# Performance work log

Measured on AMD Instinct MI355X. Metric: run time of the kernel, lower is better.

The kernel has to match this reference:

```python
import jax, jax.numpy as jnp
import numpy as np

D, H, L, P, DFF = 256, 8, 4, 4, 512
HD = D // H
SHAPES = [(128, 128), (64, 64), (32, 32), (16, 16)]


def setup_inputs() -> dict:
    key = jax.random.key(0)
    ks = jax.random.split(key, 16)
    N, Lq = 8, 1000
    Lin = sum(h * w for h, w in SHAPES)
    f = lambda k, s, sc=1.0: jax.random.normal(k, s, dtype=jnp.float32) * sc
    starts = np.cumsum([0] + [h * w for h, w in SHAPES[:-1]])
    return {
        "pre_tgt": f(ks[0], (N, Lq, D)),
        "pre_query_pos": f(ks[1], (N, Lq, D)),
        "src": f(ks[2], (N, Lin, D)),
        "pre_ref_pts": jax.random.uniform(ks[3], (N, Lq, L, 2), dtype=jnp.float32),
        "src_padding_mask": jnp.zeros((N, Lin), dtype=bool),
        "src_spatial_shapes": jnp.array(SHAPES, dtype=jnp.int32),
        "level_start_index": jnp.array(starts, dtype=jnp.int32),
        "W_value": f(ks[4], (D, D), 0.02), "b_value": jnp.zeros((D,), jnp.float32),
        "W_off": f(ks[5], (D, H * L * P * 2), 0.01), "b_off": f(ks[6], (H * L * P * 2,), 0.1),
        "W_attn": f(ks[7], (D, H * L * P), 0.02), "b_attn": jnp.zeros((H * L * P,), jnp.float32),
        "W_out": f(ks[8], (D, D), 0.02), "b_out": jnp.zeros((D,), jnp.float32),
        "g1": jnp.ones((D,), jnp.float32), "be1": jnp.zeros((D,), jnp.float32),
        "W1": f(ks[9], (D, DFF), 0.02), "b1": jnp.zeros((DFF,), jnp.float32),
        "W2": f(ks[10], (DFF, D), 0.02), "b2": jnp.zeros((D,), jnp.float32),
        "g3": jnp.ones((D,), jnp.float32), "be3": jnp.zeros((D,), jnp.float32),
    }


def layernorm(x, g, b):
    m = x.mean(-1, keepdims=True)
    v = x.var(-1, keepdims=True)
    return (x - m) * jax.lax.rsqrt(v + 1e-5) * g + b


def msdeform_attn(query, ref_pts, src, pad_mask, shapes_np,
                  W_value, b_value, W_off, b_off, W_attn, b_attn, W_out, b_out):
    N, Lq, _ = query.shape
    value = src @ W_value + b_value
    value = jnp.where(pad_mask[..., None], 0.0, value)
    value = value.reshape(N, -1, H, HD)
    off = (query @ W_off + b_off).reshape(N, Lq, H, L, P, 2)
    attn = jax.nn.softmax((query @ W_attn + b_attn).reshape(N, Lq, H, L * P), -1)
    attn = attn.reshape(N, Lq, H, L, P)
    # offset normalizer is (W, H) per level
    norm = jnp.asarray(shapes_np[:, [1, 0]], dtype=query.dtype)  # [L,2]
    loc = ref_pts[:, :, None, :, None, :] + off / norm[None, None, None, :, None, :]
    out = jnp.zeros((N, Lq, H, HD), dtype=query.dtype)
    n_idx = jnp.arange(N)[:, None, None, None]
    h_idx = jnp.arange(H)[None, None, :, None]
    start = 0
    for l in range(L):
        Hl, Wl = int(shapes_np[l, 0]), int(shapes_np[l, 1])
        vl = value[:, start:start + Hl * Wl].reshape(N, Hl, Wl, H, HD)
        start += Hl * Wl
        # grid_sample align_corners=False: pixel = loc*size - 0.5, zero padding
        x = loc[:, :, :, l, :, 0] * Wl - 0.5  # [N,Lq,H,P]
        y = loc[:, :, :, l, :, 1] * Hl - 0.5
        x0 = jnp.floor(x); y0 = jnp.floor(y)
        fx = x - x0; fy = y - y0
        x0i = x0.astype(jnp.int32); y0i = y0.astype(jnp.int32)
        samp = jnp.zeros(x.shape + (HD,), dtype=value.dtype)
        for dx, wx in ((0, 1.0 - fx), (1, fx)):
            for dy, wy in ((0, 1.0 - fy), (1, fy)):
                xi = x0i + dx; yi = y0i + dy
                valid = (xi >= 0) & (xi < Wl) & (yi >= 0) & (yi < Hl)
                v = vl[n_idx, jnp.clip(yi, 0, Hl - 1), jnp.clip(xi, 0, Wl - 1), h_idx]
                samp = samp + jnp.where(valid, wx * wy, 0.0)[..., None] * v
        out = out + jnp.einsum('nqhp,nqhpd->nqhd', attn[:, :, :, l], samp)
    return out.reshape(N, Lq, D) @ W_out + b_out


def reference(pre_tgt, pre_query_pos, src, pre_ref_pts, src_padding_mask,
              src_spatial_shapes, level_start_index,
              W_value, b_value, W_off, b_off, W_attn, b_attn, W_out, b_out,
              g1, be1, W1, b1, W2, b2, g3, be3):
    shapes_np = np.asarray(src_spatial_shapes)
    q = pre_tgt + pre_query_pos
    attn_out = msdeform_attn(q, pre_ref_pts, src, src_padding_mask, shapes_np,
                             W_value, b_value, W_off, b_off, W_attn, b_attn, W_out, b_out)
    tgt = layernorm(pre_tgt + attn_out, g1, be1)  # dropout=identity (eval)
    ff = jax.nn.relu(tgt @ W1 + b1) @ W2 + b2
    return layernorm(tgt + ff, g3, be3)
```

## Files before the change

### kernel.cpp

```cpp
#include <hip/hip_runtime.h>
#include <hip/hip_bf16.h>

#define D_MODEL 256
#define NHEAD   8
#define NLEV    4
#define NPTS    4
#define HDIM    32
#define DFFN    512
#define NBATCH  8
#define LQ      1000
#define LIN     21760
#define M_VAL   (NBATCH * LIN)
#define M_Q     (NBATCH * LQ)

typedef __attribute__((ext_vector_type(8))) short short8;
typedef __attribute__((ext_vector_type(4))) short short4v;
typedef __attribute__((ext_vector_type(4))) float f32x4;

struct alignas(8) bf16x4 { __hip_bfloat16 a, b, c, d; };

__device__ __forceinline__ short f2bf(float f) {
    __hip_bfloat16 h = __float2bfloat16(f);
    return *reinterpret_cast<short*>(&h);
}

__global__ __launch_bounds__(256)
void transpose_weights_kernel(const float* __restrict__ Wv, const float* __restrict__ Wo,
                              const float* __restrict__ W1, const float* __restrict__ W2,
                              short* __restrict__ Wv_t, short* __restrict__ Wo_t,
                              short* __restrict__ W1_t, short* __restrict__ W2_t)
{
    const int b = blockIdx.x;
    const float* src; short* dst; int K, N, tb;
    if (b < 64)       { src = Wv; dst = Wv_t; K = 256; N = 256; tb = b; }
    else if (b < 128) { src = Wo; dst = Wo_t; K = 256; N = 256; tb = b - 64; }
    else if (b < 256) { src = W1; dst = W1_t; K = 256; N = 512; tb = b - 128; }
    else              { src = W2; dst = W2_t; K = 512; N = 256; tb = b - 256; }
    const int ntn = N >> 5;
    const int kt = tb / ntn, nt = tb % ntn;
    __shared__ float t[32][33];
    const int x = threadIdx.x & 31, y = threadIdx.x >> 5;
    #pragma unroll
    for (int j = 0; j < 4; ++j)
        t[y + 8*j][x] = src[(kt*32 + y + 8*j) * N + nt*32 + x];
    __syncthreads();
    #pragma unroll
    for (int j = 0; j < 4; ++j)
        dst[(nt*32 + y + 8*j) * K + kt*32 + x] = f2bf(t[x][y + 8*j]);
}

#define BM 64
#define BN 128
#define BK 64

template<bool A_BF16, bool RELU, bool MASK, bool OUT_BF16>
__global__ __launch_bounds__(256)
void mfma_gemm_kernel(const void* __restrict__ Ain,
                      const short* __restrict__ Bt,
                      const float* __restrict__ bias,
                      const unsigned char* __restrict__ mask,
                      float* __restrict__ C, __hip_bfloat16* __restrict__ Cb,
                      int M, int N, int K)
{
    __shared__ short As[BM * BK];
    __shared__ short Bs[BN * BK];
    const int tid  = threadIdx.x;
    const int lane = tid & 63, wid = tid >> 6;
    const int wr = wid >> 1, wc = wid & 1;
    const long bm = (long)blockIdx.y * BM;
    const int  bn = blockIdx.x * BN;

    f32x4 acc[2][4];
    #pragma unroll
    for (int m = 0; m < 2; ++m)
        #pragma unroll
        for (int n = 0; n < 4; ++n)
            acc[m][n] = (f32x4){0.f, 0.f, 0.f, 0.f};

    const int ar  = tid >> 2;
    const int akq = (tid & 3) * 16;
    const int brn = tid >> 1;
    const int bkq = (tid & 1) * 32;

    for (int k0 = 0; k0 < K; k0 += BK) {
        if (!A_BF16) {
            const float* Ap = (const float*)Ain + (bm + ar) * (long)K + k0 + akq;
            #pragma unroll
            for (int i = 0; i < 4; ++i) {
                float4 v = *reinterpret_cast<const float4*>(Ap + 4*i);
                short4v s;
                s[0] = f2bf(v.x); s[1] = f2bf(v.y); s[2] = f2bf(v.z); s[3] = f2bf(v.w);
                const int e = (akq + 4*i) ^ ((ar & 7) << 3);
                *reinterpret_cast<short4v*>(&As[ar * BK + e]) = s;
            }
        } else {
            const short* Ap = (const short*)Ain + (bm + ar) * (long)K + k0 + akq;
            #pragma unroll
            for (int i = 0; i < 2; ++i) {
                short8 v = *reinterpret_cast<const short8*>(Ap + 8*i);
                const int e = (akq + 8*i) ^ ((ar & 7) << 3);
                *reinterpret_cast<short8*>(&As[ar * BK + e]) = v;
            }
        }
        {
            const short* Bp = Bt + (bn + brn) * (long)K + k0 + bkq;
            #pragma unroll
            for (int i = 0; i < 4; ++i) {
                short8 v = *reinterpret_cast<const short8*>(Bp + 8*i);
                const int e = (bkq + 8*i) ^ ((brn & 7) << 3);
                *reinterpret_cast<short8*>(&Bs[brn * BK + e]) = v;
            }
        }
        __syncthreads();
        #pragma unroll
        for (int kk = 0; kk < 2; ++kk) {
            const int kb = kk * 32 + (lane >> 4) * 8;
            short8 af[2], bfr[4];
            #pragma unroll
            for (int m = 0; m < 2; ++m) {
                const int row = wr * 32 + m * 16 + (lane & 15);
                af[m] = *reinterpret_cast<const short8*>(&As[row * BK + (kb ^ ((row & 7) << 3))]);
            }
            #pragma unroll
            for (int n = 0; n < 4; ++n) {
                const int row = wc * 64 + n * 16 + (lane & 15);
                bfr[n] = *reinterpret_cast<const short8*>(&Bs[row * BK + (kb ^ ((row & 7) << 3))]);
            }
            #pragma unroll
            for (int m = 0; m < 2; ++m)
                #pragma unroll
                for (int n = 0; n < 4; ++n)
                    acc[m][n] = __builtin_amdgcn_mfma_f32_16x16x32_bf16(af[m], bfr[n], acc[m][n], 0, 0, 0);
        }
        __syncthreads();
    }

    #pragma unroll
    for (int m = 0; m < 2; ++m) {
        #pragma unroll
        for (int n = 0; n < 4; ++n) {
            const int col = bn + wc * 64 + n * 16 + (lane & 15);
            const float bc = bias[col];
            #pragma unroll
            for (int r = 0; r < 4; ++r) {
                const long row = bm + wr * 32 + m * 16 + (lane >> 4) * 4 + r;
                float v = acc[m][n][r] + bc;
                if (RELU) v = fmaxf(v, 0.f);
                if (MASK) { if (mask[row]) v = 0.f; }
                if (OUT_BF16) Cb[row * (long)N + col] = __float2bfloat16(v);
                else          C[row * (long)N + col]  = v;
            }
        }
    }
}

template<bool ADD_A2>
__global__ __launch_bounds__(256)
void gemm_kernel(const float* __restrict__ A, const float* __restrict__ A2,
                 const float* __restrict__ B, const float* __restrict__ bias,
                 float* __restrict__ C, int M, int N, int K)
{
    __shared__ float As[16][68];
    __shared__ float Bs[16][64];
    const int tid = threadIdx.x;
    const long bm = (long)blockIdx.y * 64;
    const int  bn = blockIdx.x * 64;
    const int  tx = tid & 15, ty = tid >> 4;
    const int  ar = tid >> 2, ac = (tid & 3) * 4;

    float acc[4][4] = {};
    const float* Aptr  = A + (bm + ar) * (long)K + ac;
    const float* A2ptr = ADD_A2 ? (A2 + (bm + ar) * (long)K + ac) : nullptr;
    const float* Bptr  = B + (long)ty * N + bn + tx * 4;

    for (int k0 = 0; k0 < K; k0 += 16) {
        float4 av = *reinterpret_cast<const float4*>(Aptr + k0);
        if (ADD_A2) {
            float4 a2 = *reinterpret_cast<const float4*>(A2ptr + k0);
            av.x += a2.x; av.y += a2.y; av.z += a2.z; av.w += a2.w;
        }
        float4 bv = *reinterpret_cast<const float4*>(Bptr + (long)k0 * N);
        As[ac + 0][ar] = av.x; As[ac + 1][ar] = av.y;
        As[ac + 2][ar] = av.z; As[ac + 3][ar] = av.w;
        *reinterpret_cast<float4*>(&Bs[ty][tx * 4]) = bv;
        __syncthreads();
        #pragma unroll
        for (int kk = 0; kk < 16; ++kk) {
            float4 a4 = *reinterpret_cast<const float4*>(&As[kk][ty * 4]);
            float4 b4 = *reinterpret_cast<const float4*>(&Bs[kk][tx * 4]);
            float a[4] = {a4.x, a4.y, a4.z, a4.w};
            float b[4] = {b4.x, b4.y, b4.z, b4.w};
            #pragma unroll
            for (int i = 0; i < 4; ++i)
                #pragma unroll
                for (int j = 0; j < 4; ++j)
                    acc[i][j] = fmaf(a[i], b[j], acc[i][j]);
        }
        __syncthreads();
    }
    const float4 bias4 = *reinterpret_cast<const float4*>(bias + bn + tx * 4);
    #pragma unroll
    for (int i = 0; i < 4; ++i) {
        const long row = bm + ty * 4 + i;
        const long off = row * N + bn + tx * 4;
        *reinterpret_cast<float4*>(C + off) = make_float4(
            acc[i][0] + bias4.x, acc[i][1] + bias4.y,
            acc[i][2] + bias4.z, acc[i][3] + bias4.w);
    }
}

__global__ __launch_bounds__(128)
void msdeform_sample_kernel(const float* __restrict__ off,
                            const float* __restrict__ logits,
                            const float* __restrict__ ref_pts,
                            const __hip_bfloat16* __restrict__ value,
                            __hip_bfloat16* __restrict__ samp)
{
    const int qi = blockIdx.x;
    const int n  = qi / LQ;
    const int t  = threadIdx.x;

    __shared__ int   s_idx[128][4];
    __shared__ float s_w[128][4];

    {
        const int h = t >> 4, lp = t & 15, l = lp >> 2;
        const float lg = logits[qi * 128 + t];
        float mx = lg;
        #pragma unroll
        for (int m = 1; m < 16; m <<= 1) mx = fmaxf(mx, __shfl_xor(mx, m, 64));
        const float e = __expf(lg - mx);
        float s = e;
        #pragma unroll
        for (int m = 1; m < 16; m <<= 1) s += __shfl_xor(s, m, 64);
        const float w = e / s;

        const int Wl = 128 >> l;
        constexpr int Start[4] = {0, 16384, 20480, 21504};
        const float x = ref_pts[qi * 8 + l * 2 + 0] * (float)Wl - 0.5f
                      + off[qi * 256 + h * 32 + lp * 2 + 0];
        const float y = ref_pts[qi * 8 + l * 2 + 1] * (float)Wl - 0.5f
                      + off[qi * 256 + h * 32 + lp * 2 + 1];
        const float x0f = floorf(x), y0f = floorf(y);
        const float fx = x - x0f, fy = y - y0f;
        const int x0 = (int)x0f, y0 = (int)y0f;
        const int base = n * LIN + Start[l];
        #pragma unroll
        for (int tap = 0; tap < 4; ++tap) {
            const int dx = tap & 1, dy = tap >> 1;
            const int xi = x0 + dx, yi = y0 + dy;
            const bool ok = ((unsigned)xi < (unsigned)Wl) & ((unsigned)yi < (unsigned)Wl);
            const float tw = ok ? w * (dx ? fx : 1.f - fx) * (dy ? fy : 1.f - fy) : 0.f;
            const int idx = ok ? ((base + yi * Wl + xi) * D_MODEL + h * HDIM) : 0;
            s_idx[t][tap] = idx;
            s_w[t][tap]   = tw;
        }
    }
    __syncthreads();

    {
        const int h = t >> 4, cp = t & 15;
        float a0 = 0.f, a1 = 0.f;
        #pragma unroll
        for (int lp = 0; lp < 16; ++lp) {
            const int4   i4 = *reinterpret_cast<const int4*>(s_idx[h * 16 + lp]);
            const float4 w4 = *reinterpret_cast<const float4*>(s_w[h * 16 + lp]);
            const int   idx[4] = {i4.x, i4.y, i4.z, i4.w};
            const float wt[4]  = {w4.x, w4.y, w4.z, w4.w};
            #pragma unroll
            for (int tap = 0; tap < 4; ++tap) {
                __hip_bfloat162 v2 = *reinterpret_cast<const __hip_bfloat162*>(
                    value + idx[tap] + cp * 2);
                a0 = fmaf(wt[tap], __bfloat162float(v2.x), a0);
                a1 = fmaf(wt[tap], __bfloat162float(v2.y), a1);
            }
        }
        __hip_bfloat162 o;
        o.x = __float2bfloat16(a0);
        o.y = __float2bfloat16(a1);
        *reinterpret_cast<__hip_bfloat162*>(samp + (long)qi * D_MODEL + h * HDIM + cp * 2) = o;
    }
}

__global__ __launch_bounds__(256)
void add_ln_kernel(const float* __restrict__ x, const float* __restrict__ y,
                   const float* __restrict__ g, const float* __restrict__ b,
                   float* __restrict__ out)
{
    const int row  = blockIdx.x * 4 + (threadIdx.x >> 6);
    const int lane = threadIdx.x & 63;
    const long base = (long)row * D_MODEL + lane * 4;

    float4 xv = *reinterpret_cast<const float4*>(x + base);
    float4 yv = *reinterpret_cast<const float4*>(y + base);
    float4 v  = make_float4(xv.x + yv.x, xv.y + yv.y, xv.z + yv.z, xv.w + yv.w);

    float sum = v.x + v.y + v.z + v.w;
    float sq  = v.x * v.x + v.y * v.y + v.z * v.z + v.w * v.w;
    #pragma unroll
    for (int m = 1; m < 64; m <<= 1) {
        sum += __shfl_xor(sum, m, 64);
        sq  += __shfl_xor(sq,  m, 64);
    }
    const float mean = sum * (1.f / D_MODEL);
    const float var  = sq * (1.f / D_MODEL) - mean * mean;
    const float rstd = rsqrtf(var + 1e-5f);

    float4 gv = *reinterpret_cast<const float4*>(g + lane * 4);
    float4 bv = *reinterpret_cast<const float4*>(b + lane * 4);
    float4 o;
    o.x = (v.x - mean) * rstd * gv.x + bv.x;
    o.y = (v.y - mean) * rstd * gv.y + bv.y;
    o.z = (v.z - mean) * rstd * gv.z + bv.z;
    o.w = (v.w - mean) * rstd * gv.w + bv.w;
    *reinterpret_cast<float4*>(out + base) = o;
}

extern "C" void kernel_launch(void* const* d_in, const int* in_sizes, int n_in,
                              void* d_out, int out_size, void* d_ws, size_t ws_size,
                              hipStream_t stream)
{
    const float* pre_tgt  = (const float*)d_in[0];
    const float* pre_qpos = (const float*)d_in[1];
    const float* src      = (const float*)d_in[2];
    const float* ref_pts  = (const float*)d_in[3];
    const unsigned char* pad_mask = (const unsigned char*)d_in[4];
    const float* W_value = (const float*)d_in[7];
    const float* b_value = (const float*)d_in[8];
    const float* W_off   = (const float*)d_in[9];
    const float* b_off   = (const float*)d_in[10];
    const float* W_attn  = (const float*)d_in[11];
    const float* b_attn  = (const float*)d_in[12];
    const float* W_out   = (const float*)d_in[13];
    const float* b_out   = (const float*)d_in[14];
    const float* g1      = (const float*)d_in[15];
    const float* be1     = (const float*)d_in[16];
    const float* W1      = (const float*)d_in[17];
    const float* b1      = (const float*)d_in[18];
    const float* W2      = (const float*)d_in[19];
    const float* b2      = (const float*)d_in[20];
    const float* g3      = (const float*)d_in[21];
    const float* be3     = (const float*)d_in[22];
    float* out = (float*)d_out;

    char* w = (char*)d_ws;
    size_t o = 0;
    __hip_bfloat16* value = (__hip_bfloat16*)(w + o); o += (size_t)M_VAL * D_MODEL * 2;
    float* offb    = (float*)(w + o); o += (size_t)M_Q * 256 * 4;
    float* logits  = (float*)(w + o); o += (size_t)M_Q * 128 * 4;
    __hip_bfloat16* samp = (__hip_bfloat16*)(w + o); o += (size_t)M_Q * 256 * 2;
    float* tgt     = (float*)(w + o); o += (size_t)M_Q * 256 * 4;
    short* Wv_t    = (short*)(w + o); o += 256 * 256 * 2;
    short* Wo_t    = (short*)(w + o); o += 256 * 256 * 2;
    short* W1_t    = (short*)(w + o); o += 512 * 256 * 2;
    short* W2_t    = (short*)(w + o); o += 256 * 512 * 2;
    float* attn_out = (float*)w;
    float* hidden_f_unused = nullptr; (void)hidden_f_unused;
    __hip_bfloat16* hidden = (__hip_bfloat16*)(w + 20000000);
    float* ff = offb;

    const dim3 blk(256);

    transpose_weights_kernel<<<dim3(384), blk, 0, stream>>>(
        W_value, W_out, W1, W2, Wv_t, Wo_t, W1_t, W2_t);

    mfma_gemm_kernel<false, false, true, true><<<dim3(2, M_VAL / BM), blk, 0, stream>>>(
        src, Wv_t, b_value, pad_mask, nullptr, value, M_VAL, 256, 256);

    gemm_kernel<true><<<dim3(4, M_Q / 64), blk, 0, stream>>>(
        pre_tgt, pre_qpos, W_off, b_off, offb, M_Q, 256, 256);

    gemm_kernel<true><<<dim3(2, M_Q / 64), blk, 0, stream>>>(
        pre_tgt, pre_qpos, W_attn, b_attn, logits, M_Q, 128, 256);

    msdeform_sample_kernel<<<dim3(M_Q), dim3(128), 0, stream>>>(
        offb, logits, ref_pts, value, samp);

    mfma_gemm_kernel<true, false, false, false><<<dim3(2, M_Q / BM), blk, 0, stream>>>(
        samp, Wo_t, b_out, nullptr, attn_out, nullptr, M_Q, 256, 256);

    add_ln_kernel<<<dim3(M_Q / 4), blk, 0, stream>>>(pre_tgt, attn_out, g1, be1, tgt);

    mfma_gemm_kernel<false, true, false, true><<<dim3(4, M_Q / BM), blk, 0, stream>>>(
        tgt, W1_t, b1, nullptr, nullptr, hidden, M_Q, 512, 256);

    mfma_gemm_kernel<true, false, false, false><<<dim3(2, M_Q / BM), blk, 0, stream>>>(
        hidden, W2_t, b2, nullptr, ff, nullptr, M_Q, 256, 512);

    add_ln_kernel<<<dim3(M_Q / 4), blk, 0, stream>>>(tgt, ff, g3, be3, out);
}
```

Measured before the change: 434.4 us.

## Head-major value layout, clamped bilinear gather, fused offset/attn GEMM, register prefetch

The value projection now writes a head-major layout [H][N*Lin][32], so each head's samples sit in a contiguous region. The sampling kernel clamps the 2x2 footprint inside the level and folds out-of-range taps into zero weights, which gives two contiguous 8-byte loads per point instead of four scattered 4-byte ones. The offset and attention-logit fp32 GEMMs are merged into one launch, and both GEMM kernels prefetch the next K tile into registers while computing the current one. The risks are higher register pressure, strided bf16 stores in the value GEMM epilogue, and extra branching in the weight setup.

```diff
diff --git a/kernel.cpp b/kernel.cpp
--- a/kernel.cpp
+++ b/kernel.cpp
@@ -23,6 +23,9 @@
     __hip_bfloat16 h = __float2bfloat16(f);
     return *reinterpret_cast<short*>(&h);
 }
+__device__ __forceinline__ float bf2f(short s) {
+    return __uint_as_float(((unsigned)(unsigned short)s) << 16);
+}
 
 __global__ __launch_bounds__(256)
 void transpose_weights_kernel(const float* __restrict__ Wv, const float* __restrict__ Wo,
@@ -53,7 +56,7 @@
 #define BN 128
 #define BK 64
 
-template<bool A_BF16, bool RELU, bool MASK, bool OUT_BF16>
+template<bool A_BF16, bool RELU, bool MASK, int OMODE>
 __global__ __launch_bounds__(256)
 void mfma_gemm_kernel(const void* __restrict__ Ain,
                       const short* __restrict__ Bt,
@@ -82,36 +85,52 @@
     const int brn = tid >> 1;
     const int bkq = (tid & 1) * 32;
 
-    for (int k0 = 0; k0 < K; k0 += BK) {
+    float4 a_f[4];
+    short8 a_h[2];
+    short8 b_r[4];
+
+    auto load_tile = [&](int k0) {
         if (!A_BF16) {
             const float* Ap = (const float*)Ain + (bm + ar) * (long)K + k0 + akq;
             #pragma unroll
+            for (int i = 0; i < 4; ++i)
+                a_f[i] = *reinterpret_cast<const float4*>(Ap + 4*i);
+        } else {
+            const short* Ap = (const short*)Ain + (bm + ar) * (long)K + k0 + akq;
+            #pragma unroll
+            for (int i = 0; i < 2; ++i)
+                a_h[i] = *reinterpret_cast<const short8*>(Ap + 8*i);
+        }
+        const short* Bp = Bt + (bn + brn) * (long)K + k0 + bkq;
+        #pragma unroll
+        for (int i = 0; i < 4; ++i)
+            b_r[i] = *reinterpret_cast<const short8*>(Bp + 8*i);
+    };
+    auto store_tile = [&]() {
+        if (!A_BF16) {
+            #pragma unroll
             for (int i = 0; i < 4; ++i) {
-                float4 v = *reinterpret_cast<const float4*>(Ap + 4*i);
                 short4v s;
-                s[0] = f2bf(v.x); s[1] = f2bf(v.y); s[2] = f2bf(v.z); s[3] = f2bf(v.w);
-                const int e = (akq + 4*i) ^ ((ar & 7) << 3);
-                *reinterpret_cast<short4v*>(&As[ar * BK + e]) = s;
+                s[0] = f2bf(a_f[i].x); s[1] = f2bf(a_f[i].y);
+                s[2] = f2bf(a_f[i].z); s[3] = f2bf(a_f[i].w);
+                *reinterpret_cast<short4v*>(&As[ar * BK + ((akq + 4*i) ^ ((ar & 7) << 3))]) = s;
             }
         } else {
-            const short* Ap = (const short*)Ain + (bm + ar) * (long)K + k0 + akq;
-            #pragma unroll
-            for (int i = 0; i < 2; ++i) {
-                short8 v = *reinterpret_cast<const short8*>(Ap + 8*i);
-                const int e = (akq + 8*i) ^ ((ar & 7) << 3);
-                *reinterpret_cast<short8*>(&As[ar * BK + e]) = v;
-            }
-        }
-        {
-            const short* Bp = Bt + (bn + brn) * (long)K + k0 + bkq;
-            #pragma unroll
-            for (int i = 0; i < 4; ++i) {
-                short8 v = *reinterpret_cast<const short8*>(Bp + 8*i);
-                const int e = (bkq + 8*i) ^ ((brn & 7) << 3);
-                *reinterpret_cast<short8*>(&Bs[brn * BK + e]) = v;
-            }
-        }
+            #pragma unroll
+            for (int i = 0; i < 2; ++i)
+                *reinterpret_cast<short8*>(&As[ar * BK + ((akq + 8*i) ^ ((ar & 7) << 3))]) = a_h[i];
+        }
+        #pragma unroll
+        for (int i = 0; i < 4; ++i)
+            *reinterpret_cast<short8*>(&Bs[brn * BK + ((bkq + 8*i) ^ ((brn & 7) << 3))]) = b_r[i];
+    };
+
+    load_tile(0);
+    const int nsteps = K / BK;
+    for (int s = 0; s < nsteps; ++s) {
+        store_tile();
         __syncthreads();
+        if (s + 1 < nsteps) load_tile((s + 1) * BK);
         #pragma unroll
         for (int kk = 0; kk < 2; ++kk) {
             const int kb = kk * 32 + (lane >> 4) * 8;
@@ -147,43 +166,54 @@
                 float v = acc[m][n][r] + bc;
                 if (RELU) v = fmaxf(v, 0.f);
                 if (MASK) { if (mask[row]) v = 0.f; }
-                if (OUT_BF16) Cb[row * (long)N + col] = __float2bfloat16(v);
-                else          C[row * (long)N + col]  = v;
+                if (OMODE == 0)      C[row * (long)N + col] = v;
+                else if (OMODE == 1) Cb[row * (long)N + col] = __float2bfloat16(v);
+                else {
+                    Cb[(size_t)(col >> 5) * ((size_t)M_VAL * HDIM)
+                       + (size_t)row * HDIM + (col & 31)] = __float2bfloat16(v);
+                }
             }
         }
     }
 }
 
-template<bool ADD_A2>
 __global__ __launch_bounds__(256)
-void gemm_kernel(const float* __restrict__ A, const float* __restrict__ A2,
-                 const float* __restrict__ B, const float* __restrict__ bias,
-                 float* __restrict__ C, int M, int N, int K)
+void proj_gemm_kernel(const float* __restrict__ A, const float* __restrict__ A2,
+                      const float* __restrict__ Wo, const float* __restrict__ bo,
+                      const float* __restrict__ Wa, const float* __restrict__ ba,
+                      float* __restrict__ Co, float* __restrict__ Ca)
 {
     __shared__ float As[16][68];
     __shared__ float Bs[16][64];
     const int tid = threadIdx.x;
     const long bm = (long)blockIdx.y * 64;
     const int  bn = blockIdx.x * 64;
-    const int  tx = tid & 15, ty = tid >> 4;
-    const int  ar = tid >> 2, ac = (tid & 3) * 4;
-
+    const float* B; const float* bias; float* C; int Nc, cb;
+    if (bn < 256) { B = Wo; bias = bo; C = Co; Nc = 256; cb = bn; }
+    else          { B = Wa; bias = ba; C = Ca; Nc = 128; cb = bn - 256; }
+
+    const int tx = tid & 15, ty = tid >> 4;
+    const int ar = tid >> 2, ac = (tid & 3) * 4;
     float acc[4][4] = {};
-    const float* Aptr  = A + (bm + ar) * (long)K + ac;
-    const float* A2ptr = ADD_A2 ? (A2 + (bm + ar) * (long)K + ac) : nullptr;
-    const float* Bptr  = B + (long)ty * N + bn + tx * 4;
-
-    for (int k0 = 0; k0 < K; k0 += 16) {
-        float4 av = *reinterpret_cast<const float4*>(Aptr + k0);
-        if (ADD_A2) {
-            float4 a2 = *reinterpret_cast<const float4*>(A2ptr + k0);
-            av.x += a2.x; av.y += a2.y; av.z += a2.z; av.w += a2.w;
-        }
-        float4 bv = *reinterpret_cast<const float4*>(Bptr + (long)k0 * N);
-        As[ac + 0][ar] = av.x; As[ac + 1][ar] = av.y;
-        As[ac + 2][ar] = av.z; As[ac + 3][ar] = av.w;
+    const float* Aptr = A  + (bm + ar) * 256L + ac;
+    const float* A2p  = A2 + (bm + ar) * 256L + ac;
+    const float* Bptr = B + (long)ty * Nc + cb + tx * 4;
+
+    float4 av, a2, bv;
+    auto load = [&](int k0) {
+        av = *reinterpret_cast<const float4*>(Aptr + k0);
+        a2 = *reinterpret_cast<const float4*>(A2p + k0);
+        bv = *reinterpret_cast<const float4*>(Bptr + (long)k0 * Nc);
+    };
+    load(0);
+    for (int k0 = 0; k0 < 256; k0 += 16) {
+        As[ac + 0][ar] = av.x + a2.x;
+        As[ac + 1][ar] = av.y + a2.y;
+        As[ac + 2][ar] = av.z + a2.z;
+        As[ac + 3][ar] = av.w + a2.w;
         *reinterpret_cast<float4*>(&Bs[ty][tx * 4]) = bv;
         __syncthreads();
+        if (k0 + 16 < 256) load(k0 + 16);
         #pragma unroll
         for (int kk = 0; kk < 16; ++kk) {
             float4 a4 = *reinterpret_cast<const float4*>(&As[kk][ty * 4]);
@@ -198,12 +228,11 @@
         }
         __syncthreads();
     }
-    const float4 bias4 = *reinterpret_cast<const float4*>(bias + bn + tx * 4);
+    const float4 bias4 = *reinterpret_cast<const float4*>(bias + cb + tx * 4);
     #pragma unroll
     for (int i = 0; i < 4; ++i) {
         const long row = bm + ty * 4 + i;
-        const long off = row * N + bn + tx * 4;
-        *reinterpret_cast<float4*>(C + off) = make_float4(
+        *reinterpret_cast<float4*>(C + row * Nc + cb + tx * 4) = make_float4(
             acc[i][0] + bias4.x, acc[i][1] + bias4.y,
             acc[i][2] + bias4.z, acc[i][3] + bias4.w);
     }
@@ -220,8 +249,9 @@
     const int n  = qi / LQ;
     const int t  = threadIdx.x;
 
-    __shared__ int   s_idx[128][4];
-    __shared__ float s_w[128][4];
+    __shared__ int   s_base[128];
+    __shared__ float s_wx[128][2];
+    __shared__ float s_wy[128][2];
 
     {
         const int h = t >> 4, lp = t & 15, l = lp >> 2;
@@ -230,10 +260,10 @@
         #pragma unroll
         for (int m = 1; m < 16; m <<= 1) mx = fmaxf(mx, __shfl_xor(mx, m, 64));
         const float e = __expf(lg - mx);
-        float s = e;
-        #pragma unroll
-        for (int m = 1; m < 16; m <<= 1) s += __shfl_xor(s, m, 64);
-        const float w = e / s;
+        float ssum = e;
+        #pragma unroll
+        for (int m = 1; m < 16; m <<= 1) ssum += __shfl_xor(ssum, m, 64);
+        const float w = e / ssum;
 
         const int Wl = 128 >> l;
         constexpr int Start[4] = {0, 16384, 20480, 21504};
@@ -241,44 +271,51 @@
                       + off[qi * 256 + h * 32 + lp * 2 + 0];
         const float y = ref_pts[qi * 8 + l * 2 + 1] * (float)Wl - 0.5f
                       + off[qi * 256 + h * 32 + lp * 2 + 1];
-        const float x0f = floorf(x), y0f = floorf(y);
-        const float fx = x - x0f, fy = y - y0f;
-        const int x0 = (int)x0f, y0 = (int)y0f;
-        const int base = n * LIN + Start[l];
-        #pragma unroll
-        for (int tap = 0; tap < 4; ++tap) {
-            const int dx = tap & 1, dy = tap >> 1;
-            const int xi = x0 + dx, yi = y0 + dy;
-            const bool ok = ((unsigned)xi < (unsigned)Wl) & ((unsigned)yi < (unsigned)Wl);
-            const float tw = ok ? w * (dx ? fx : 1.f - fx) * (dy ? fy : 1.f - fy) : 0.f;
-            const int idx = ok ? ((base + yi * Wl + xi) * D_MODEL + h * HDIM) : 0;
-            s_idx[t][tap] = idx;
-            s_w[t][tap]   = tw;
-        }
+        const float xf = floorf(x), yf = floorf(y);
+        const float fx = x - xf, fy = y - yf;
+        const int x0 = (int)xf, y0 = (int)yf;
+        const int xb = min(max(x0, 0), Wl - 2);
+        const int yb = min(max(y0, 0), Wl - 2);
+        const float wx0 = (xb == x0) ? (1.f - fx) : ((xb == x0 + 1) ? fx : 0.f);
+        const float wx1 = (xb + 1 == x0) ? (1.f - fx) : ((xb == x0) ? fx : 0.f);
+        const float wy0 = w * ((yb == y0) ? (1.f - fy) : ((yb == y0 + 1) ? fy : 0.f));
+        const float wy1 = w * ((yb + 1 == y0) ? (1.f - fy) : ((yb == y0) ? fy : 0.f));
+
+        const int row = n * LIN + Start[l] + yb * Wl + xb;
+        s_base[t]  = (h * M_VAL + row) * HDIM;
+        s_wx[t][0] = wx0; s_wx[t][1] = wx1;
+        s_wy[t][0] = wy0; s_wy[t][1] = wy1;
     }
     __syncthreads();
 
     {
         const int h = t >> 4, cp = t & 15;
-        float a0 = 0.f, a1 = 0.f;
+        const int side = cp >> 3, ch4 = (cp & 7) * 4;
+        float a0 = 0.f, a1 = 0.f, a2 = 0.f, a3 = 0.f;
         #pragma unroll
         for (int lp = 0; lp < 16; ++lp) {
-            const int4   i4 = *reinterpret_cast<const int4*>(s_idx[h * 16 + lp]);
-            const float4 w4 = *reinterpret_cast<const float4*>(s_w[h * 16 + lp]);
-            const int   idx[4] = {i4.x, i4.y, i4.z, i4.w};
-            const float wt[4]  = {w4.x, w4.y, w4.z, w4.w};
-            #pragma unroll
-            for (int tap = 0; tap < 4; ++tap) {
-                __hip_bfloat162 v2 = *reinterpret_cast<const __hip_bfloat162*>(
-                    value + idx[tap] + cp * 2);
-                a0 = fmaf(wt[tap], __bfloat162float(v2.x), a0);
-                a1 = fmaf(wt[tap], __bfloat162float(v2.y), a1);
-            }
-        }
-        __hip_bfloat162 o;
-        o.x = __float2bfloat16(a0);
-        o.y = __float2bfloat16(a1);
-        *reinterpret_cast<__hip_bfloat162*>(samp + (long)qi * D_MODEL + h * HDIM + cp * 2) = o;
+            const int i  = h * 16 + lp;
+            const int rs = (128 >> (lp >> 2)) * HDIM;
+            const int b  = s_base[i] + side * HDIM + ch4;
+            const float wxs = s_wx[i][side];
+            const float w0 = wxs * s_wy[i][0];
+            const float w1 = wxs * s_wy[i][1];
+            const short4v v0 = *reinterpret_cast<const short4v*>(value + b);
+            const short4v v1 = *reinterpret_cast<const short4v*>(value + b + rs);
+            a0 += w0 * bf2f(v0[0]) + w1 * bf2f(v1[0]);
+            a1 += w0 * bf2f(v0[1]) + w1 * bf2f(v1[1]);
+            a2 += w0 * bf2f(v0[2]) + w1 * bf2f(v1[2]);
+            a3 += w0 * bf2f(v0[3]) + w1 * bf2f(v1[3]);
+        }
+        a0 += __shfl_xor(a0, 8, 64);
+        a1 += __shfl_xor(a1, 8, 64);
+        a2 += __shfl_xor(a2, 8, 64);
+        a3 += __shfl_xor(a3, 8, 64);
+        if (side == 0) {
+            bf16x4 o { __float2bfloat16(a0), __float2bfloat16(a1),
+                       __float2bfloat16(a2), __float2bfloat16(a3) };
+            *reinterpret_cast<bf16x4*>(samp + (long)qi * D_MODEL + h * HDIM + ch4) = o;
+        }
     }
 }
 
@@ -355,7 +392,6 @@
     short* W1_t    = (short*)(w + o); o += 512 * 256 * 2;
     short* W2_t    = (short*)(w + o); o += 256 * 512 * 2;
     float* attn_out = (float*)w;
-    float* hidden_f_unused = nullptr; (void)hidden_f_unused;
     __hip_bfloat16* hidden = (__hip_bfloat16*)(w + 20000000);
     float* ff = offb;
 
@@ -364,27 +400,24 @@
     transpose_weights_kernel<<<dim3(384), blk, 0, stream>>>(
         W_value, W_out, W1, W2, Wv_t, Wo_t, W1_t, W2_t);
 
-    mfma_gemm_kernel<false, false, true, true><<<dim3(2, M_VAL / BM), blk, 0, stream>>>(
+    mfma_gemm_kernel<false, false, true, 2><<<dim3(2, M_VAL / BM), blk, 0, stream>>>(
         src, Wv_t, b_value, pad_mask, nullptr, value, M_VAL, 256, 256);
 
-    gemm_kernel<true><<<dim3(4, M_Q / 64), blk, 0, stream>>>(
-        pre_tgt, pre_qpos, W_off, b_off, offb, M_Q, 256, 256);
-
-    gemm_kernel<true><<<dim3(2, M_Q / 64), blk, 0, stream>>>(
-        pre_tgt, pre_qpos, W_attn, b_attn, logits, M_Q, 128, 256);
+    proj_gemm_kernel<<<dim3(6, M_Q / 64), blk, 0, stream>>>(
+        pre_tgt, pre_qpos, W_off, b_off, W_attn, b_attn, offb, logits);
 
     msdeform_sample_kernel<<<dim3(M_Q), dim3(128), 0, stream>>>(
         offb, logits, ref_pts, value, samp);
 
-    mfma_gemm_kernel<true, false, false, false><<<dim3(2, M_Q / BM), blk, 0, stream>>>(
+    mfma_gemm_kernel<true, false, false, 0><<<dim3(2, M_Q / BM), blk, 0, stream>>>(
         samp, Wo_t, b_out, nullptr, attn_out, nullptr, M_Q, 256, 256);
 
     add_ln_kernel<<<dim3(M_Q / 4), blk, 0, stream>>>(pre_tgt, attn_out, g1, be1, tgt);
 
-    mfma_gemm_kernel<false, true, false, true><<<dim3(4, M_Q / BM), blk, 0, stream>>>(
+    mfma_gemm_kernel<false, true, false, 1><<<dim3(4, M_Q / BM), blk, 0, stream>>>(
         tgt, W1_t, b1, nullptr, nullptr, hidden, M_Q, 512, 256);
 
-    mfma_gemm_kernel<true, false, false, false><<<dim3(2, M_Q / BM), blk, 0, stream>>>(
+    mfma_gemm_kernel<true, false, false, 0><<<dim3(2, M_Q / BM), blk, 0, stream>>>(
         hidden, W2_t, b2, nullptr, ff, nullptr, M_Q, 256, 512);
 
     add_ln_kernel<<<dim3(M_Q / 4), blk, 0, stream>>>(tgt, ff, g3, be3, out);
```

Measured after the change: 418.5 us. -3.6%, faster.
